# Kernel tuning notes

Measured on AMD Instinct MI355X. Metric: run time of the kernel, lower is better.

## Reference

```python
import jax, jax.numpy as jnp
import numpy as np

B, C, H, W = 32, 1, 28, 896
WW = WS = 28
S = (W - WW) // WS + 1  # 32 windows
CONV_DIM, FC_DIM, NUM_CLASSES = 64, 128, 83
FC_IN = CONV_DIM * (H // 2) * (WW // 2)  # 64*14*14 = 12544


def setup_inputs() -> dict:
    key = jax.random.key(0)
    ks = jax.random.split(key, 9)
    sc = 0.05
    return {
        "x": jax.random.normal(ks[0], (B, C, H, W), jnp.float32),
        "conv1_w": jax.random.normal(ks[1], (CONV_DIM, C, 3, 3), jnp.float32) * sc,
        "conv1_b": jax.random.normal(ks[2], (CONV_DIM,), jnp.float32) * sc,
        "conv2_w": jax.random.normal(ks[3], (CONV_DIM, CONV_DIM, 3, 3), jnp.float32) * sc,
        "conv2_b": jax.random.normal(ks[4], (CONV_DIM,), jnp.float32) * sc,
        "fc1_w": jax.random.normal(ks[5], (FC_DIM, FC_IN), jnp.float32) * sc,
        "fc1_b": jax.random.normal(ks[6], (FC_DIM,), jnp.float32) * sc,
        "fc2_w": jax.random.normal(ks[7], (NUM_CLASSES, FC_DIM), jnp.float32) * sc,
        "fc2_b": jax.random.normal(ks[8], (NUM_CLASSES,), jnp.float32) * sc,
    }


def _conv_relu(x, w, b):
    # 3x3 conv, stride 1, padding 1 (torch Conv2d padding=1), then ReLU
    y = jax.lax.conv_general_dilated(
        x, w, window_strides=(1, 1), padding=((1, 1), (1, 1)),
        dimension_numbers=("NCHW", "OIHW", "NCHW"))
    return jax.nn.relu(y + b[None, :, None, None])


def reference(x, conv1_w, conv1_b, conv2_w, conv2_b, fc1_w, fc1_b, fc2_w, fc2_b):
    Bx = x.shape[0]
    # WS == WW -> non-overlapping windows; extract all S windows at once via reshape
    # (B, C, H, S*WW) -> (B*S, C, H, WW)
    win = x.reshape(Bx, C, H, S, WW).transpose(0, 3, 1, 2, 4).reshape(Bx * S, C, H, WW)
    h = _conv_relu(win, conv1_w, conv1_b)
    h = _conv_relu(h, conv2_w, conv2_b)
    # MaxPool2d(2)
    h = jax.lax.reduce_window(h, -jnp.inf, jax.lax.max,
                              window_dimensions=(1, 1, 2, 2),
                              window_strides=(1, 1, 2, 2), padding="VALID")
    # dropout is identity in eval mode
    h = h.reshape(Bx * S, FC_IN)  # torch.flatten(x, 1) on NCHW matches row-major reshape
    h = jax.nn.relu(h @ fc1_w.T + fc1_b)
    logits = h @ fc2_w.T + fc2_b  # (B*S, num_classes)
    # -> (B, num_classes, S) as in the torch module
    return logits.reshape(Bx, S, NUM_CLASSES).transpose(0, 2, 1)
```

## Files before the change

kernel.cpp:

```cpp
#include <hip/hip_runtime.h>
#include <hip/hip_bf16.h>


typedef __attribute__((ext_vector_type(8))) short short8;
typedef __attribute__((ext_vector_type(4))) float f32x4;
typedef __attribute__((ext_vector_type(16))) float f32x16;

#define WB1_E   0u
#define WB2_E   2048u
#define WFC1_E  38912u
#define WFC2_E  1644544u
#define POOL_E  1656832u
#define PART_B  29003776u

__device__ __forceinline__ unsigned short f2bf(float f) {
  unsigned u = __float_as_uint(f);
  u += 0x7fffu + ((u >> 16) & 1u);
  return (unsigned short)(u >> 16);
}
__device__ __forceinline__ unsigned cvtpk_bf16(float a, float b) {
  unsigned r;
  asm("v_cvt_pk_bf16_f32 %0, %1, %2" : "=v"(r) : "v"(a), "v"(b));
  return r;
}

__global__ __launch_bounds__(256) void prep_kernel(
    const float* __restrict__ w1, const float* __restrict__ c1b,
    const float* __restrict__ w2, const float* __restrict__ wfc1,
    const float* __restrict__ wfc2, unsigned short* __restrict__ ws16)
{
  int i = blockIdx.x * blockDim.x + threadIdx.x;
  if (i < 2048) {
    int j = i & 7, l = (i >> 3) & 63, nt = i >> 9;
    int n = nt * 16 + (l & 15), k = 8 * (l >> 4) + j;
    float v = (k < 9) ? w1[n * 9 + k] : (k == 9 ? c1b[n] : 0.f);
    ws16[WB1_E + i] = f2bf(v);
  } else if (i < 38912) {
    int i2 = i - 2048;
    int j = i2 & 7, l = (i2 >> 3) & 63, rest = i2 >> 9;
    int ks = rest % 36, nh = rest / 36;
    int co = nh * 32 + (l & 31);
    int k = ks * 16 + (l >> 5) * 8 + j;
    int dydx = k >> 6, ci = k & 63;
    ws16[WB2_E + i2] = f2bf(w2[co * 576 + ci * 9 + dydx]);
  } else if (i < 1644544) {
    int i2 = i - 38912;
    int j = i2 & 7, l = (i2 >> 3) & 63, rest = i2 >> 9;
    int ks = rest % 392, nt = rest / 392;
    int fcn = nt * 16 + (l & 15);
    int kp = ks * 32 + 8 * (l >> 4) + j;
    int co = kp & 63, r2 = kp >> 6;
    int oxp = r2 % 14, oyp = r2 / 14;
    ws16[WFC1_E + i2] = f2bf(wfc1[fcn * 12544 + co * 196 + oyp * 14 + oxp]);
  } else if (i < 1656832) {
    int i2 = i - 1644544;
    int j = i2 & 7, l = (i2 >> 3) & 63, rest = i2 >> 9;
    int ks = rest & 3, nt = rest >> 2;
    int cls = nt * 16 + (l & 15);
    int k = ks * 32 + 8 * (l >> 4) + j;
    float v = (cls < 83) ? wfc2[cls * 128 + k] : 0.f;
    ws16[WFC2_E + i2] = f2bf(v);
  }
}

__global__ __launch_bounds__(512, 4) void conv_kernel(
    const float* __restrict__ x, const float* __restrict__ c2b,
    unsigned short* __restrict__ ws16)
{
  extern __shared__ char smem[];
  unsigned short* xw = (unsigned short*)(smem + 77760);

  const int tid = threadIdx.x;
  const int wave = tid >> 6, lane = tid & 63;
  const int bid = blockIdx.x;
  const int n = bid >> 1, hf = bid & 1;
  const int rlo = hf ? 15 : 0;
  const int M1 = hf ? 364 : 476;
  const int T1 = hf ? 23 : 30;
  const int lr_off = hf ? -15 : 1;

  const short8* wb1 = (const short8*)(ws16 + WB1_E);
  unsigned short* poolg = ws16 + POOL_E + (unsigned)n * 12544u;

  short8 z8 = {0, 0, 0, 0, 0, 0, 0, 0};
  {
    short8* l8 = (short8*)smem;
    for (int idx = tid; idx < 4860; idx += 512) l8[idx] = z8;
    const float* xg = x + (n >> 5) * 25088 + (n & 31) * 28;
    for (int i = tid; i < 900; i += 512) {
      int yy = (i * 2185) >> 16;
      int xx = i - yy * 30;
      int iy = yy - 1, ix = xx - 1;
      bool inb = (iy >= 0) && (iy < 28) && (ix >= 0) && (ix < 28);
      float v = inb ? xg[iy * 896 + ix] : 0.f;
      xw[i] = f2bf(v);
    }
  }
  __syncthreads();

  {
    const int g = lane >> 4, l15 = lane & 15;
    short8 b1f[4];
#pragma unroll
    for (int nt = 0; nt < 4; ++nt) b1f[nt] = wb1[nt * 64 + lane];
    for (int mt = wave; mt < T1; mt += 8) {
      int m = mt * 16 + l15;
      bool mval = m < M1;
      int mc = mval ? m : M1 - 1;
      int yr = (mc * 2341) >> 16;
      int rr = rlo + yr;
      int ox = mc - yr * 28;
      const char* xb = (const char*)xw + (rr * 30 + ox) * 2;
      short8 a = z8;
      if (g == 0) {
        a[0] = *(const short*)(xb + 0);
        a[1] = *(const short*)(xb + 2);
        a[2] = *(const short*)(xb + 4);
        a[3] = *(const short*)(xb + 60);
        a[4] = *(const short*)(xb + 62);
        a[5] = *(const short*)(xb + 64);
        a[6] = *(const short*)(xb + 120);
        a[7] = *(const short*)(xb + 122);
      } else if (g == 1) {
        a[0] = *(const short*)(xb + 124);
        a[1] = (short)0x3F80;
      }
      f32x4 d[4];
#pragma unroll
      for (int nt = 0; nt < 4; ++nt) {
        f32x4 zz = {0.f, 0.f, 0.f, 0.f};
        d[nt] = __builtin_amdgcn_mfma_f32_16x16x32_bf16(b1f[nt], a, zz, 0, 0, 0);
      }
      if (mval) {
        int spB = ((rr + lr_off) * 30 + ox + 1) * 144;
#pragma unroll
        for (int nt = 0; nt < 4; ++nt) {
          float r0 = fmaxf(d[nt][0], 0.f), r1 = fmaxf(d[nt][1], 0.f);
          float r2 = fmaxf(d[nt][2], 0.f), r3 = fmaxf(d[nt][3], 0.f);
          int co2 = nt * 16 + 4 * g;
          *(unsigned*)(smem + (spB + co2 * 2)) = cvtpk_bf16(r0, r1);
          *(unsigned*)(smem + (spB + co2 * 2 + 4)) = cvtpk_bf16(r2, r3);
        }
      }
    }
  }
  __syncthreads();

  {
    const int l31 = lane & 31;
    const int h = lane >> 5;
    const int T32 = hf ? 11 : 14;
    const int Wh  = hf ? 84 : 112;
    const float bias0 = c2b[l31];
    const float bias1 = c2b[32 + l31];
    const short8* wb2w = (const short8*)(ws16 + WB2_E) + lane;

    const bool v1 = (wave + 8) < T32;
    int baseB0, baseB1;
    {
      int lw = wave * 8 + (l31 >> 2);
      int py = lw / 14, px = lw % 14;
      baseB0 = ((2 * py + ((l31 >> 1) & 1)) * 30 + 2 * px + (l31 & 1)) * 144 + h * 16;
      int tI1 = v1 ? (wave + 8) : wave;
      int lw1 = tI1 * 8 + (l31 >> 2);
      int py1 = lw1 / 14, px1 = lw1 % 14;
      baseB1 = ((2 * py1 + ((l31 >> 1) & 1)) * 30 + 2 * px1 + (l31 & 1)) * 144 + h * 16;
    }
    f32x16 acc00 = (f32x16)(0.0f), acc01 = (f32x16)(0.0f);
    f32x16 acc10 = (f32x16)(0.0f), acc11 = (f32x16)(0.0f);

    short8 bfA0, bfA1, bfA2, bfA3;
    short8 bfB0, bfB1, bfB2, bfB3;

#define LOADB(d0, d1, d2, d3, hp) do {                                   \
      const int ph_ = (hp) >> 1, k0_ = ((hp) & 1) * 2;                   \
      d0 = wb2w[(ph_ * 4 + k0_) * 64];                                   \
      d1 = wb2w[(ph_ * 4 + k0_ + 1) * 64];                               \
      d2 = wb2w[2304 + (ph_ * 4 + k0_) * 64];                            \
      d3 = wb2w[2304 + (ph_ * 4 + k0_ + 1) * 64];                        \
    } while (0)
#define COMPT(hp, base, aL, aH, b0, b1, b2, b3) do {                     \
      const int ph_ = (hp) >> 1, k0_ = ((hp) & 1) * 2;                   \
      const int cell_ = ((ph_ / 3) * 30 + (ph_ % 3)) * 144 + 32 * k0_;   \
      short8 a0 = *(const short8*)(smem + (base + cell_));               \
      short8 a1 = *(const short8*)(smem + (base + cell_ + 32));          \
      aL = __builtin_amdgcn_mfma_f32_32x32x16_bf16(a0, b0, aL, 0, 0, 0); \
      aH = __builtin_amdgcn_mfma_f32_32x32x16_bf16(a0, b2, aH, 0, 0, 0); \
      aL = __builtin_amdgcn_mfma_f32_32x32x16_bf16(a1, b1, aL, 0, 0, 0); \
      aH = __builtin_amdgcn_mfma_f32_32x32x16_bf16(a1, b3, aH, 0, 0, 0); \
    } while (0)

    LOADB(bfA0, bfA1, bfA2, bfA3, 0);
    if (v1) {
#pragma unroll
      for (int hp = 0; hp < 18; hp += 2) {
        __builtin_amdgcn_s_barrier();
        if (hp + 1 < 18) LOADB(bfB0, bfB1, bfB2, bfB3, hp + 1);
        COMPT(hp, baseB0, acc00, acc01, bfA0, bfA1, bfA2, bfA3);
        COMPT(hp, baseB1, acc10, acc11, bfA0, bfA1, bfA2, bfA3);
        if (hp + 2 < 18) LOADB(bfA0, bfA1, bfA2, bfA3, hp + 2);
        COMPT(hp + 1, baseB0, acc00, acc01, bfB0, bfB1, bfB2, bfB3);
        COMPT(hp + 1, baseB1, acc10, acc11, bfB0, bfB1, bfB2, bfB3);
      }
    } else {
#pragma unroll
      for (int hp = 0; hp < 18; hp += 2) {
        __builtin_amdgcn_s_barrier();
        if (hp + 1 < 18) LOADB(bfB0, bfB1, bfB2, bfB3, hp + 1);
        COMPT(hp, baseB0, acc00, acc01, bfA0, bfA1, bfA2, bfA3);
        if (hp + 2 < 18) LOADB(bfA0, bfA1, bfA2, bfA3, hp + 2);
        COMPT(hp + 1, baseB0, acc00, acc01, bfB0, bfB1, bfB2, bfB3);
      }
    }
#undef LOADB
#undef COMPT

#pragma unroll
    for (int q = 0; q < 4; ++q) {
      int lw0 = wave * 8 + 2 * q + h;
      {
        float p0 = fmaxf(fmaxf(acc00[4 * q], acc00[4 * q + 1]),
                         fmaxf(acc00[4 * q + 2], acc00[4 * q + 3]));
        float p1 = fmaxf(fmaxf(acc01[4 * q], acc01[4 * q + 1]),
                         fmaxf(acc01[4 * q + 2], acc01[4 * q + 3]));
        unsigned pk = cvtpk_bf16(fmaxf(p0 + bias0, 0.f), fmaxf(p1 + bias1, 0.f));
        poolg[(hf * 112 + lw0) * 64 + l31]      = (unsigned short)pk;
        poolg[(hf * 112 + lw0) * 64 + 32 + l31] = (unsigned short)(pk >> 16);
      }
      if (v1) {
        int lw1 = (wave + 8) * 8 + 2 * q + h;
        if (lw1 < Wh) {
          float p0 = fmaxf(fmaxf(acc10[4 * q], acc10[4 * q + 1]),
                           fmaxf(acc10[4 * q + 2], acc10[4 * q + 3]));
          float p1 = fmaxf(fmaxf(acc11[4 * q], acc11[4 * q + 1]),
                           fmaxf(acc11[4 * q + 2], acc11[4 * q + 3]));
          unsigned pk = cvtpk_bf16(fmaxf(p0 + bias0, 0.f), fmaxf(p1 + bias1, 0.f));
          poolg[(hf * 112 + lw1) * 64 + l31]      = (unsigned short)pk;
          poolg[(hf * 112 + lw1) * 64 + 32 + l31] = (unsigned short)(pk >> 16);
        }
      }
    }
  }
}

__global__ __launch_bounds__(512) void fc1_kernel(unsigned short* __restrict__ ws16)
{
  extern __shared__ char smem[];
  short8* A8 = (short8*)smem;
  const int tid = threadIdx.x;
  const int wave = tid >> 6, lane = tid & 63;
  const int g = lane >> 4, l15 = lane & 15;
  const int ig = blockIdx.x >> 2, q = blockIdx.x & 3;
  const short8* pool8 = (const short8*)(ws16 + POOL_E);
  const short8* wf1 = (const short8*)(ws16 + WFC1_E);
  {
    int img = tid >> 5, l32 = tid & 31;
    const short8* src = pool8 + (ig * 16 + img) * 1568 + q * 392;
#pragma unroll
    for (int j = 0; j < 13; ++j) {
      int idx = l32 + 32 * j;
      if (idx < 392) A8[img * 393 + idx] = src[idx];
    }
  }
  __syncthreads();
  f32x4 accA = {0.f, 0.f, 0.f, 0.f}, accB = {0.f, 0.f, 0.f, 0.f};
  const short8* wbase = wf1 + (wave * 392 + q * 98) * 64 + lane;
  short8 b0 = wbase[0 * 64], b1 = wbase[1 * 64], b2 = wbase[2 * 64], b3 = wbase[3 * 64];
  short8 b4 = wbase[4 * 64], b5 = wbase[5 * 64], b6 = wbase[6 * 64], b7 = wbase[7 * 64];
#pragma unroll 1
  for (int c = 0; c < 12; ++c) {
    int ks = 8 * c;
    short8 a;
    a = A8[l15 * 393 + (ks + 0) * 4 + g];
    accA = __builtin_amdgcn_mfma_f32_16x16x32_bf16(a, b0, accA, 0, 0, 0);
    b0 = wbase[(ks + 8) * 64];
    a = A8[l15 * 393 + (ks + 1) * 4 + g];
    accB = __builtin_amdgcn_mfma_f32_16x16x32_bf16(a, b1, accB, 0, 0, 0);
    b1 = wbase[(ks + 9) * 64];
    a = A8[l15 * 393 + (ks + 2) * 4 + g];
    accA = __builtin_amdgcn_mfma_f32_16x16x32_bf16(a, b2, accA, 0, 0, 0);
    b2 = wbase[(ks + 10) * 64];
    a = A8[l15 * 393 + (ks + 3) * 4 + g];
    accB = __builtin_amdgcn_mfma_f32_16x16x32_bf16(a, b3, accB, 0, 0, 0);
    b3 = wbase[(ks + 11) * 64];
    a = A8[l15 * 393 + (ks + 4) * 4 + g];
    accA = __builtin_amdgcn_mfma_f32_16x16x32_bf16(a, b4, accA, 0, 0, 0);
    b4 = wbase[(ks + 12) * 64];
    a = A8[l15 * 393 + (ks + 5) * 4 + g];
    accB = __builtin_amdgcn_mfma_f32_16x16x32_bf16(a, b5, accB, 0, 0, 0);
    b5 = wbase[(ks + 13) * 64];
    a = A8[l15 * 393 + (ks + 6) * 4 + g];
    accA = __builtin_amdgcn_mfma_f32_16x16x32_bf16(a, b6, accA, 0, 0, 0);
    b6 = wbase[(ks + 14) * 64];
    a = A8[l15 * 393 + (ks + 7) * 4 + g];
    accB = __builtin_amdgcn_mfma_f32_16x16x32_bf16(a, b7, accB, 0, 0, 0);
    b7 = wbase[(ks + 15) * 64];
  }
  {
    short8 a;
    a = A8[l15 * 393 + 96 * 4 + g];
    accA = __builtin_amdgcn_mfma_f32_16x16x32_bf16(a, b0, accA, 0, 0, 0);
    a = A8[l15 * 393 + 97 * 4 + g];
    accB = __builtin_amdgcn_mfma_f32_16x16x32_bf16(a, b1, accB, 0, 0, 0);
  }
  _Float16* part = (_Float16*)((char*)ws16 + PART_B);
  int base = ((q * 64 + ig) * 16 + 4 * g) * 128 + wave * 16 + l15;
#pragma unroll
  for (int i = 0; i < 4; ++i) part[base + i * 128] = (_Float16)(accA[i] + accB[i]);
}

__global__ __launch_bounds__(512) void fc2_kernel(
    const float* __restrict__ b1, const float* __restrict__ b2,
    const unsigned short* __restrict__ ws16, float* __restrict__ out)
{
  __shared__ unsigned short h_s[16 * 136];
  const int tid = threadIdx.x;
  const int wave = tid >> 6, lane = tid & 63;
  const int g = lane >> 4, l15 = lane & 15;
  const int ig = blockIdx.x;
  const _Float16* part = (const _Float16*)((const char*)ws16 + PART_B);
#pragma unroll
  for (int t = 0; t < 4; ++t) {
    int u = tid + 512 * t;
    int img = u >> 7, fcn = u & 127;
    float s = 0.f;
#pragma unroll
    for (int q2 = 0; q2 < 4; ++q2)
      s += (float)part[((q2 * 64 + ig) * 16 + img) * 128 + fcn];
    h_s[img * 136 + fcn] = f2bf(fmaxf(s + b1[fcn], 0.f));
  }
  __syncthreads();
  if (wave < 6) {
    const short8* wf2 = (const short8*)(ws16 + WFC2_E);
    const short8* h8 = (const short8*)h_s;
    f32x4 a2 = {0.f, 0.f, 0.f, 0.f};
#pragma unroll
    for (int ks = 0; ks < 4; ++ks) {
      short8 b = wf2[(wave * 4 + ks) * 64 + lane];
      short8 a = h8[l15 * 17 + ks * 4 + g];
      a2 = __builtin_amdgcn_mfma_f32_16x16x32_bf16(a, b, a2, 0, 0, 0);
    }
    int cls = wave * 16 + l15;
    if (cls < 83) {
      float bias2 = b2[cls];
#pragma unroll
      for (int i = 0; i < 4; ++i) {
        int nimg = ig * 16 + 4 * g + i;
        out[((nimg >> 5) * 83 + cls) * 32 + (nimg & 31)] = a2[i] + bias2;
      }
    }
  }
}

extern "C" void kernel_launch(void* const* d_in, const int* in_sizes, int n_in,
                              void* d_out, int out_size, void* d_ws, size_t ws_size,
                              hipStream_t stream)
{
  const float* x    = (const float*)d_in[0];
  const float* w1   = (const float*)d_in[1];
  const float* c1b  = (const float*)d_in[2];
  const float* w2   = (const float*)d_in[3];
  const float* c2b  = (const float*)d_in[4];
  const float* wfc1 = (const float*)d_in[5];
  const float* bfc1 = (const float*)d_in[6];
  const float* wfc2 = (const float*)d_in[7];
  const float* bfc2 = (const float*)d_in[8];
  unsigned short* ws16 = (unsigned short*)d_ws;
  float* out = (float*)d_out;

  prep_kernel<<<6472, 256, 0, stream>>>(w1, c1b, w2, wfc1, wfc2, ws16);
  conv_kernel<<<2048, 512, 79616, stream>>>(x, c2b, ws16);
  fc1_kernel<<<256, 512, 100608, stream>>>(ws16);
  fc2_kernel<<<64, 512, 0, stream>>>(bfc1, bfc2, ws16, out);
}
```

Measured before the change: 91.47 us.

## Coalesce fc1 weight repack via LDS transpose and zero only halo cells

The fc1 weight conversion to bf16 MFMA layout now loads contiguous source rows into shared memory and writes 16-byte packed outputs, replacing scattered per-element gathers. The prep grid shrinks from 6472 to 312 blocks. The conv kernel now zeroes only the border cells of the padded conv1 output tile instead of clearing the whole LDS region, which removes redundant LDS stores. This relies on the interior being fully overwritten later, and the transpose reads from LDS may hit bank conflicts.

```diff
diff --git a/kernel.cpp b/kernel.cpp
--- a/kernel.cpp
+++ b/kernel.cpp
@@ -29,37 +29,59 @@
     const float* __restrict__ w2, const float* __restrict__ wfc1,
     const float* __restrict__ wfc2, unsigned short* __restrict__ ws16)
 {
-  int i = blockIdx.x * blockDim.x + threadIdx.x;
-  if (i < 2048) {
-    int j = i & 7, l = (i >> 3) & 63, nt = i >> 9;
-    int n = nt * 16 + (l & 15), k = 8 * (l >> 4) + j;
-    float v = (k < 9) ? w1[n * 9 + k] : (k == 9 ? c1b[n] : 0.f);
-    ws16[WB1_E + i] = f2bf(v);
-  } else if (i < 38912) {
-    int i2 = i - 2048;
-    int j = i2 & 7, l = (i2 >> 3) & 63, rest = i2 >> 9;
-    int ks = rest % 36, nh = rest / 36;
-    int co = nh * 32 + (l & 31);
-    int k = ks * 16 + (l >> 5) * 8 + j;
-    int dydx = k >> 6, ci = k & 63;
-    ws16[WB2_E + i2] = f2bf(w2[co * 576 + ci * 9 + dydx]);
-  } else if (i < 1644544) {
-    int i2 = i - 38912;
-    int j = i2 & 7, l = (i2 >> 3) & 63, rest = i2 >> 9;
-    int ks = rest % 392, nt = rest / 392;
-    int fcn = nt * 16 + (l & 15);
-    int kp = ks * 32 + 8 * (l >> 4) + j;
-    int co = kp & 63, r2 = kp >> 6;
-    int oxp = r2 % 14, oyp = r2 / 14;
-    ws16[WFC1_E + i2] = f2bf(wfc1[fcn * 12544 + co * 196 + oyp * 14 + oxp]);
-  } else if (i < 1656832) {
-    int i2 = i - 1644544;
-    int j = i2 & 7, l = (i2 >> 3) & 63, rest = i2 >> 9;
-    int ks = rest & 3, nt = rest >> 2;
-    int cls = nt * 16 + (l & 15);
-    int k = ks * 32 + 8 * (l >> 4) + j;
-    float v = (cls < 83) ? wfc2[cls * 128 + k] : 0.f;
-    ws16[WFC2_E + i2] = f2bf(v);
+  const int b = blockIdx.x, tid = threadIdx.x;
+  if (b < 112) {
+    __shared__ unsigned short T[14336];
+    const int nt = b / 14, ksc = b % 14;
+    const float* src = wfc1 + nt * 16 * 12544 + 14 * ksc;
+#pragma unroll
+    for (int it = 0; it < 56; ++it) {
+      int u = tid + 256 * it;
+      int f = u / 896;
+      int rem = u - f * 896;
+      int co = rem / 14;
+      int sp = rem - co * 14;
+      T[u] = f2bf(src[f * 12544 + co * 196 + sp]);
+    }
+    __syncthreads();
+    unsigned short* dst = ws16 + WFC1_E + (unsigned)(nt * 392 + 28 * ksc) * 512u;
+#pragma unroll
+    for (int it = 0; it < 7; ++it) {
+      int v = tid + 256 * it;
+      int ksl = v >> 6, l = v & 63;
+      int f15 = l & 15, g = l >> 4;
+      int co0 = ((ksl & 1) << 5) + 8 * g;
+      int spl = ksl >> 1;
+      short8 o;
+#pragma unroll
+      for (int j = 0; j < 8; ++j)
+        o[j] = (short)T[f15 * 896 + (co0 + j) * 14 + spl];
+      *(short8*)(dst + v * 8) = o;
+    }
+  } else {
+    int u = (b - 112) * 256 + tid;
+    if (u < 2048) {
+      int j = u & 7, l = (u >> 3) & 63, nt = u >> 9;
+      int n = nt * 16 + (l & 15), k = 8 * (l >> 4) + j;
+      float v = (k < 9) ? w1[n * 9 + k] : (k == 9 ? c1b[n] : 0.f);
+      ws16[WB1_E + u] = f2bf(v);
+    } else if (u < 38912) {
+      int i2 = u - 2048;
+      int j = i2 & 7, l = (i2 >> 3) & 63, rest = i2 >> 9;
+      int ks = rest % 36, nh = rest / 36;
+      int co = nh * 32 + (l & 31);
+      int k = ks * 16 + (l >> 5) * 8 + j;
+      int dydx = k >> 6, ci = k & 63;
+      ws16[WB2_E + i2] = f2bf(w2[co * 576 + ci * 9 + dydx]);
+    } else {
+      int i2 = u - 38912;
+      int j = i2 & 7, l = (i2 >> 3) & 63, rest = i2 >> 9;
+      int ks = rest & 3, nt = rest >> 2;
+      int cls = nt * 16 + (l & 15);
+      int k = ks * 32 + 8 * (l >> 4) + j;
+      float v = (cls < 83) ? wfc2[cls * 128 + k] : 0.f;
+      ws16[WFC2_E + i2] = f2bf(v);
+    }
   }
 }
 
@@ -84,8 +106,19 @@
 
   short8 z8 = {0, 0, 0, 0, 0, 0, 0, 0};
   {
-    short8* l8 = (short8*)smem;
-    for (int idx = tid; idx < 4860; idx += 512) l8[idx] = z8;
+    int cell = tid >> 3, e = tid & 7;
+    int r, c;
+    if (hf == 0) {
+      if (cell < 30)      { r = 0;         c = cell; }
+      else if (cell < 47) { r = cell - 29; c = 0; }
+      else                { r = cell - 46; c = 29; }
+    } else {
+      if (cell < 30)      { r = 13;        c = cell; }
+      else if (cell < 43) { r = cell - 30; c = 0; }
+      else if (cell < 56) { r = cell - 43; c = 29; }
+      else                { r = 13;        c = 0; }
+    }
+    *(short8*)(smem + ((r * 30 + c) * 144 + e * 16)) = z8;
     const float* xg = x + (n >> 5) * 25088 + (n & 31) * 28;
     for (int i = tid; i < 900; i += 512) {
       int yy = (i * 2185) >> 16;
@@ -368,7 +401,7 @@
   unsigned short* ws16 = (unsigned short*)d_ws;
   float* out = (float*)d_out;
 
-  prep_kernel<<<6472, 256, 0, stream>>>(w1, c1b, w2, wfc1, wfc2, ws16);
+  prep_kernel<<<312, 256, 0, stream>>>(w1, c1b, w2, wfc1, wfc2, ws16);
   conv_kernel<<<2048, 512, 79616, stream>>>(x, c2b, ws16);
   fc1_kernel<<<256, 512, 100608, stream>>>(ws16);
   fc2_kernel<<<64, 512, 0, stream>>>(bfc1, bfc2, ws16, out);
```

New measurement: 90.45 us. About the same (-1.1%).
